# Optimization experiments

Hardware: AMD Instinct MI355X
Metric: run time of the kernel (lower is better)

The kernel has to match this reference:

```python
import jax, jax.numpy as jnp
import numpy as np

NUM_FIELDS = 40
EMBED = 64
# pair indices (i<j) matching itertools.combinations order
_I, _J = np.triu_indices(NUM_FIELDS, k=1)
NUM_PAIRS = _I.shape[0]  # 780


def setup_inputs() -> dict:
    key = jax.random.key(0)
    k1, k2 = jax.random.split(key)
    feature_emb = jax.random.normal(k1, (2048, NUM_FIELDS, EMBED), dtype=jnp.float32)
    bound = 1.0 / np.sqrt(EMBED)  # nn.Linear default init range
    W = jax.random.uniform(k2, (NUM_PAIRS, EMBED, EMBED), dtype=jnp.float32,
                           minval=-bound, maxval=bound)
    return {"feature_emb": feature_emb, "W": W}


def reference(feature_emb, W):
    # field_interaction: for pair p=(i,j): (v_i @ W_p^T) * v_j
    idx_i = jnp.asarray(_I)
    idx_j = jnp.asarray(_J)
    vi = feature_emb[:, idx_i, :]  # [B, P, E]
    vj = feature_emb[:, idx_j, :]  # [B, P, E]
    # nn.Linear: y = x @ W^T  -> einsum over input-feature axis e
    out = jnp.einsum('bpe,pfe->bpf', vi, W) * vj  # [B, P, E]
    return out
```

## Files before the change

### kernel.cpp

```cpp
#include <hip/hip_runtime.h>

#define NUM_FIELDS 40
#define NPAIRS     780
#define EMBED      64
#define BATCH      2048
#define BB         64
#define PT         26
#define NBC        (BATCH/BB)
#define NPC        (NPAIRS/PT)
#define NBLK       (NBC*NPC)

typedef __attribute__((ext_vector_type(8))) short bf16x8;
typedef __attribute__((ext_vector_type(4))) short short4v;
typedef __attribute__((ext_vector_type(4))) float f32x4;

__device__ __forceinline__ short f2bf(float f) {
    unsigned u = __builtin_bit_cast(unsigned, f);
    u += 0x7FFFu + ((u >> 16) & 1u);
    return (short)(u >> 16);
}

__global__ __launch_bounds__(256, 4)
void bilinear_mfma2(const float* __restrict__ emb,
                    const float* __restrict__ Wg,
                    float* __restrict__ out) {
    __shared__ __align__(16) short WbS[2][64][8][8];
    __shared__ __align__(16) short VIS[64][8][8];

    const int bid  = blockIdx.x;
    const int orig = (bid & 7) * (NBLK / 8) + (bid >> 3);
    const int bc   = orig % NBC;
    const int pc   = orig / NBC;
    const int bblk = bc * BB;
    const int p0   = pc * PT;

    const int t = threadIdx.x;

    int fi = 0, rem = p0, cnt = NUM_FIELDS - 1;
    while (rem >= cnt) { rem -= cnt; --cnt; ++fi; }
    int fj = fi + 1 + rem;

    {
        const float4* Wp = (const float4*)(Wg + (size_t)p0 * EMBED * EMBED);
        #pragma unroll
        for (int k = 0; k < 4; ++k) {
            int n = t + 256 * k;
            int row = n >> 4, e4 = n & 15;
            float4 wv = Wp[n];
            float4 vv = *(const float4*)(emb +
                          ((size_t)(bblk + row) * NUM_FIELDS + fi) * EMBED + e4 * 4);
            int o = e4 >> 1, half = e4 & 1;
            int slot = o ^ (row & 7);
            short4v cw, cv;
            cw.x = f2bf(wv.x); cw.y = f2bf(wv.y); cw.z = f2bf(wv.z); cw.w = f2bf(wv.w);
            cv.x = f2bf(vv.x); cv.y = f2bf(vv.y); cv.z = f2bf(vv.z); cv.w = f2bf(vv.w);
            *(short4v*)&WbS[0][row][slot][half * 4] = cw;
            *(short4v*)&VIS[row][slot][half * 4] = cv;
        }
    }
    __syncthreads();

    const int w   = t >> 6;
    const int l   = t & 63;
    const int l15 = l & 15;
    const int l4  = l >> 4;

    const size_t bg    = (size_t)(bblk + 16 * w + l15);
    const float* vjbase = emb + bg * NUM_FIELDS * EMBED;
    float*       obase  = out + (bg * NPAIRS) * (size_t)EMBED;

    for (int pi = 0; pi < PT; ++pi) {
        const int cur = pi & 1, nxt = cur ^ 1;
        const int p   = p0 + pi;

        int fi_n = fi, fj_n = fj + 1;
        if (fj_n == NUM_FIELDS) { fi_n = fi + 1; fj_n = fi_n + 1; }

        const bool havenext  = (pi + 1 < PT);
        const bool fi_change = havenext && (fi_n != fi);

        float4 Wpre[4], Vpre[4];
        if (havenext) {
            const float4* Wp = (const float4*)(Wg + (size_t)(p + 1) * EMBED * EMBED);
            #pragma unroll
            for (int k = 0; k < 4; ++k) {
                int n = t + 256 * k;
                Wpre[k] = Wp[n];
            }
        }
        if (fi_change) {
            #pragma unroll
            for (int k = 0; k < 4; ++k) {
                int n = t + 256 * k;
                int row = n >> 4, e4 = n & 15;
                Vpre[k] = *(const float4*)(emb +
                            ((size_t)(bblk + row) * NUM_FIELDS + fi_n) * EMBED + e4 * 4);
            }
        }

        const float* vjrow = vjbase + (size_t)fj * EMBED;
        float4 vj4[4];
        #pragma unroll
        for (int nt = 0; nt < 4; ++nt)
            vj4[nt] = *(const float4*)(vjrow + nt * 16 + l4 * 4);

        bf16x8 bfr[2];
        #pragma unroll
        for (int kk = 0; kk < 2; ++kk) {
            int row  = 16 * w + l15;
            int slot = (kk * 4 + l4) ^ (row & 7);
            bfr[kk] = *(const bf16x8*)&VIS[row][slot][0];
        }

        f32x4 acc[4];
        #pragma unroll
        for (int nt = 0; nt < 4; ++nt) {
            acc[nt].x = 0.f; acc[nt].y = 0.f; acc[nt].z = 0.f; acc[nt].w = 0.f;
            #pragma unroll
            for (int kk = 0; kk < 2; ++kk) {
                int row  = 16 * nt + l15;
                int slot = (kk * 4 + l4) ^ (row & 7);
                bf16x8 afr = *(const bf16x8*)&WbS[cur][row][slot][0];
                acc[nt] = __builtin_amdgcn_mfma_f32_16x16x32_bf16(afr, bfr[kk], acc[nt], 0, 0, 0);
            }
        }

        float* orow = obase + (size_t)p * EMBED;
        #pragma unroll
        for (int nt = 0; nt < 4; ++nt) {
            f32x4 o;
            o.x = acc[nt].x * vj4[nt].x;
            o.y = acc[nt].y * vj4[nt].y;
            o.z = acc[nt].z * vj4[nt].z;
            o.w = acc[nt].w * vj4[nt].w;
            __builtin_nontemporal_store(o, (f32x4*)(orow + nt * 16 + l4 * 4));
        }

        if (havenext) {
            #pragma unroll
            for (int k = 0; k < 4; ++k) {
                int n = t + 256 * k;
                int row = n >> 4, e4 = n & 15;
                int o = e4 >> 1, half = e4 & 1;
                int slot = o ^ (row & 7);
                short4v cw;
                cw.x = f2bf(Wpre[k].x); cw.y = f2bf(Wpre[k].y);
                cw.z = f2bf(Wpre[k].z); cw.w = f2bf(Wpre[k].w);
                *(short4v*)&WbS[nxt][row][slot][half * 4] = cw;
            }
        }
        if (fi_change) {
            __syncthreads();
            #pragma unroll
            for (int k = 0; k < 4; ++k) {
                int n = t + 256 * k;
                int row = n >> 4, e4 = n & 15;
                int o = e4 >> 1, half = e4 & 1;
                int slot = o ^ (row & 7);
                short4v cv;
                cv.x = f2bf(Vpre[k].x); cv.y = f2bf(Vpre[k].y);
                cv.z = f2bf(Vpre[k].z); cv.w = f2bf(Vpre[k].w);
                *(short4v*)&VIS[row][slot][half * 4] = cv;
            }
        }

        fi = fi_n; fj = fj_n;
        __syncthreads();
    }
}

extern "C" void kernel_launch(void* const* d_in, const int* in_sizes, int n_in,
                              void* d_out, int out_size, void* d_ws, size_t ws_size,
                              hipStream_t stream) {
    const float* emb = (const float*)d_in[0];
    const float* W   = (const float*)d_in[1];
    float*       out = (float*)d_out;

    hipLaunchKernelGGL(bilinear_mfma2, dim3(NBLK), dim3(256), 0, stream, emb, W, out);
}
```

Before: 162.3 us.

## Pre-convert W and embeddings to bf16, load MFMA fragments directly from global

```diff
diff --git a/kernel.cpp b/kernel.cpp
--- a/kernel.cpp
+++ b/kernel.cpp
@@ -10,6 +10,9 @@
 #define NPC        (NPAIRS/PT)
 #define NBLK       (NBC*NPC)
 
+#define NW_ELEMS   (NPAIRS*EMBED*EMBED)
+#define NE_ELEMS   (BATCH*NUM_FIELDS*EMBED)
+
 typedef __attribute__((ext_vector_type(8))) short bf16x8;
 typedef __attribute__((ext_vector_type(4))) short short4v;
 typedef __attribute__((ext_vector_type(4))) float f32x4;
@@ -18,6 +21,102 @@
     unsigned u = __builtin_bit_cast(unsigned, f);
     u += 0x7FFFu + ((u >> 16) & 1u);
     return (short)(u >> 16);
+}
+
+__global__ __launch_bounds__(256)
+void cvt_to_bf16(const float* __restrict__ src, short* __restrict__ dst, int n8) {
+    for (int i = blockIdx.x * 256 + threadIdx.x; i < n8; i += gridDim.x * 256) {
+        const float4* s = (const float4*)src + 2 * (size_t)i;
+        float4 a = s[0], b = s[1];
+        short4v lo, hi;
+        lo.x = f2bf(a.x); lo.y = f2bf(a.y); lo.z = f2bf(a.z); lo.w = f2bf(a.w);
+        hi.x = f2bf(b.x); hi.y = f2bf(b.y); hi.z = f2bf(b.z); hi.w = f2bf(b.w);
+        ((short4v*)dst)[2 * (size_t)i]     = lo;
+        ((short4v*)dst)[2 * (size_t)i + 1] = hi;
+    }
+}
+
+__global__ __launch_bounds__(256)
+void bilinear_direct(const short* __restrict__ Wbf,
+                     const short* __restrict__ embbf,
+                     const float* __restrict__ emb,
+                     float* __restrict__ out) {
+    const int bid  = blockIdx.x;
+    const int orig = (bid & 7) * (NBLK / 8) + (bid >> 3);
+    const int bc   = orig % NBC;
+    const int pc   = orig / NBC;
+    const int bblk = bc * BB;
+    const int p0   = pc * PT;
+
+    const int t   = threadIdx.x;
+    const int w   = t >> 6;
+    const int l   = t & 63;
+    const int l15 = l & 15;
+    const int l4  = l >> 4;
+
+    int fi = 0, rem = p0, cnt = NUM_FIELDS - 1;
+    while (rem >= cnt) { rem -= cnt; --cnt; ++fi; }
+    int fj = fi + 1 + rem;
+
+    const int    bg     = bblk + 16 * w + l15;
+    const float* vjbase = emb + (size_t)bg * NUM_FIELDS * EMBED;
+    const short* vibase = embbf + (size_t)bg * NUM_FIELDS * EMBED + l4 * 8;
+
+    bf16x8 bfr[2];
+    {
+        const short* vib = vibase + (size_t)fi * EMBED;
+        bfr[0] = *(const bf16x8*)(vib);
+        bfr[1] = *(const bf16x8*)(vib + 32);
+    }
+
+    const short* wb = Wbf + (size_t)p0 * (EMBED * EMBED) + l15 * EMBED + l4 * 8;
+
+    #pragma unroll 2
+    for (int pi = 0; pi < PT; ++pi) {
+        const int p = p0 + pi;
+        const short* wp = wb + (size_t)pi * (EMBED * EMBED);
+
+        bf16x8 afr[8];
+        #pragma unroll
+        for (int nt = 0; nt < 4; ++nt) {
+            afr[2 * nt]     = *(const bf16x8*)(wp + nt * 16 * EMBED);
+            afr[2 * nt + 1] = *(const bf16x8*)(wp + nt * 16 * EMBED + 32);
+        }
+
+        const float* vjrow = vjbase + (size_t)fj * EMBED;
+        float4 vj4[4];
+        #pragma unroll
+        for (int nt = 0; nt < 4; ++nt)
+            vj4[nt] = *(const float4*)(vjrow + nt * 16 + l4 * 4);
+
+        f32x4 acc[4];
+        #pragma unroll
+        for (int nt = 0; nt < 4; ++nt) {
+            acc[nt].x = 0.f; acc[nt].y = 0.f; acc[nt].z = 0.f; acc[nt].w = 0.f;
+            acc[nt] = __builtin_amdgcn_mfma_f32_16x16x32_bf16(afr[2 * nt],     bfr[0], acc[nt], 0, 0, 0);
+            acc[nt] = __builtin_amdgcn_mfma_f32_16x16x32_bf16(afr[2 * nt + 1], bfr[1], acc[nt], 0, 0, 0);
+        }
+
+        float* orow = out + ((size_t)bg * NPAIRS + p) * EMBED;
+        #pragma unroll
+        for (int nt = 0; nt < 4; ++nt) {
+            f32x4 o;
+            o.x = acc[nt].x * vj4[nt].x;
+            o.y = acc[nt].y * vj4[nt].y;
+            o.z = acc[nt].z * vj4[nt].z;
+            o.w = acc[nt].w * vj4[nt].w;
+            __builtin_nontemporal_store(o, (f32x4*)(orow + nt * 16 + l4 * 4));
+        }
+
+        int fi_n = fi, fj_n = fj + 1;
+        if (fj_n == NUM_FIELDS) { fi_n = fi + 1; fj_n = fi_n + 1; }
+        if (fi_n != fi) {
+            const short* vib = vibase + (size_t)fi_n * EMBED;
+            bfr[0] = *(const bf16x8*)(vib);
+            bfr[1] = *(const bf16x8*)(vib + 32);
+        }
+        fi = fi_n; fj = fj_n;
+    }
 }
 
 __global__ __launch_bounds__(256, 4)
@@ -33,7 +132,6 @@
     const int pc   = orig / NBC;
     const int bblk = bc * BB;
     const int p0   = pc * PT;
-
     const int t = threadIdx.x;
 
     int fi = 0, rem = p0, cnt = NUM_FIELDS - 1;
@@ -60,22 +158,16 @@
     }
     __syncthreads();
 
-    const int w   = t >> 6;
-    const int l   = t & 63;
-    const int l15 = l & 15;
-    const int l4  = l >> 4;
-
-    const size_t bg    = (size_t)(bblk + 16 * w + l15);
+    const int w = t >> 6, l = t & 63, l15 = l & 15, l4 = l >> 4;
+    const size_t bg = (size_t)(bblk + 16 * w + l15);
     const float* vjbase = emb + bg * NUM_FIELDS * EMBED;
     float*       obase  = out + (bg * NPAIRS) * (size_t)EMBED;
 
     for (int pi = 0; pi < PT; ++pi) {
         const int cur = pi & 1, nxt = cur ^ 1;
         const int p   = p0 + pi;
-
         int fi_n = fi, fj_n = fj + 1;
         if (fj_n == NUM_FIELDS) { fi_n = fi + 1; fj_n = fi_n + 1; }
-
         const bool havenext  = (pi + 1 < PT);
         const bool fi_change = havenext && (fi_n != fi);
 
@@ -83,10 +175,7 @@
         if (havenext) {
             const float4* Wp = (const float4*)(Wg + (size_t)(p + 1) * EMBED * EMBED);
             #pragma unroll
-            for (int k = 0; k < 4; ++k) {
-                int n = t + 256 * k;
-                Wpre[k] = Wp[n];
-            }
+            for (int k = 0; k < 4; ++k) Wpre[k] = Wp[t + 256 * k];
         }
         if (fi_change) {
             #pragma unroll
@@ -176,5 +265,15 @@
     const float* W   = (const float*)d_in[1];
     float*       out = (float*)d_out;
 
-    hipLaunchKernelGGL(bilinear_mfma2, dim3(NBLK), dim3(256), 0, stream, emb, W, out);
-}
+    const size_t need = (size_t)(NW_ELEMS + NE_ELEMS) * sizeof(short);
+    if (ws_size >= need) {
+        short* Wbf   = (short*)d_ws;
+        short* embbf = Wbf + NW_ELEMS;
+        const int nw8 = NW_ELEMS / 8, ne8 = NE_ELEMS / 8;
+        hipLaunchKernelGGL(cvt_to_bf16, dim3((nw8 + 255) / 256), dim3(256), 0, stream, W,   Wbf,   nw8);
+        hipLaunchKernelGGL(cvt_to_bf16, dim3((ne8 + 255) / 256), dim3(256), 0, stream, emb, embbf, ne8);
+        hipLaunchKernelGGL(bilinear_direct, dim3(NBLK), dim3(256), 0, stream, Wbf, embbf, emb, out);
+    } else {
+        hipLaunchKernelGGL(bilinear_mfma2, dim3(NBLK), dim3(256), 0, stream, emb, W, out);
+    }
+}
```

Measured after the change: 181.9 us. 1.12x slower.
